# Kernel optimization log

Hardware: AMD Instinct MI355X
Metric: run time of the kernel (lower is better)

The kernel has to match this reference:

```python
import jax, jax.numpy as jnp
import numpy as np

N_POINTS = 65536      # total nodes across the batch
NDIMS = 3
NUM_THETAS = 64       # directions
BUMP_STEPS = 32       # discretization steps of [-radius, radius]
NUM_GRAPHS = 64       # number of point clouds in the batch
RADIUS = 1.1
SCALE = 100.0         # sigmoid sharpness


def setup_inputs() -> dict:
    key = jax.random.key(0)
    k1, k2, k3 = jax.random.split(key, 3)
    x = jax.random.normal(k1, (N_POINTS, NDIMS), dtype=jnp.float32)
    # unit-norm direction vectors on the sphere, columns of v: [ndims, num_thetas]
    v = jax.random.normal(k2, (NDIMS, NUM_THETAS), dtype=jnp.float32)
    v = v / jnp.linalg.norm(v, axis=0, keepdims=True)
    # lin = discretization of [-radius, radius], matches nn.Parameter linspace
    lin = jnp.linspace(-RADIUS, RADIUS, BUMP_STEPS, dtype=jnp.float32)
    # sorted batch index assigning each node to a graph (torch_geometric convention)
    batch = jnp.sort(jax.random.randint(k3, (N_POINTS,), 0, NUM_GRAPHS, dtype=jnp.int32))
    return {"x": x, "v": v, "lin": lin, "batch": batch}


def reference(x, v, lin, batch):
    # node heights: inner product of coordinates with each direction -> [N, T]
    nh = x @ v
    # broadcast soft-threshold: sigmoid(scale * (lin - nh)) -> [N, S, T]
    # (torch builds [S,1,N,T] then movedims to [N,1,S,T]; same values)
    ecc = jax.nn.sigmoid(SCALE * (lin[None, :, None] - nh[:, None, :]))
    # segment scatter-add over nodes per graph -> [B, S, T]
    ect = jax.ops.segment_sum(ecc, batch, num_segments=NUM_GRAPHS)
    return ect  # torch output after .squeeze(): [batch, bump_steps, num_thetas]
```

## Files before the change

kernel.cpp:

```cpp
#include <hip/hip_runtime.h>

#define T      64
#define S      32
#define NGRAPH 64
#define NSPLIT 16
#define NW     4
#define XCAP   128

__global__ __launch_bounds__(256, 4) void ect_partial(
    const float* __restrict__ x, const float* __restrict__ v,
    const float* __restrict__ lin, const int* __restrict__ batch,
    float* __restrict__ out, int n_points)
{
    __shared__ float bins[2][32][128];
    __shared__ float x4[XCAP * 4];

    const int tid  = threadIdx.x;
    const int t    = tid & 63;
    const int w    = __builtin_amdgcn_readfirstlane(tid >> 6);
    const int half = w >> 1;
    const int col  = ((w & 1) << 6) + t;
    float* bw = &bins[half][0][0];
    const int b    = blockIdx.x;
    const int g    = b >> 4;
    const int c    = b & (NSPLIT - 1);

    {
        const float4 z4 = {0.0f, 0.0f, 0.0f, 0.0f};
        float4* b4 = (float4*)&bins[0][0][0];
#pragma unroll
        for (int i = 0; i < 8; i++) b4[tid + i * 256] = z4;
    }

    const int target = (t < 32) ? g : (g + 1);
    const int i32    = t & 31;
    int lo = 0;
    const int strides[3] = {2048, 64, 2};
#pragma unroll
    for (int rnd = 0; rnd < 3; rnd++) {
        const int stride = strides[rnd];
        const int idx  = lo + i32 * stride;
        const int pv   = batch[min(idx, n_points - 1)];
        const bool prd = (idx < n_points) && (pv < target);
        const unsigned long long bal = __ballot(prd);
        const int cnt = __popc((unsigned)(bal >> (t & 32)));
        lo += max(cnt - 1, 0) * stride;
    }
    if ((lo < n_points) && (batch[min(lo, n_points - 1)] < target)) lo++;
    const int gstart = __builtin_amdgcn_readfirstlane(lo);
    const int gend   = __builtin_amdgcn_readlane(lo, 32);
    const int len    = gend - gstart;
    const int n0     = gstart + (len * c) / NSPLIT;
    const int n1     = gstart + (len * (c + 1)) / NSPLIT;
    const int sliceLen = n1 - n0;

    {
        const int limit = 3 * min(sliceLen, XCAP);
        const int base3 = 3 * n0;
        for (int p = tid; p < limit; p += 256) {
            const int n = p / 3;
            const int d = p - 3 * n;
            x4[n * 4 + d] = x[base3 + p];
        }
    }

    const float lin0     = lin[0];
    const float step     = lin[1] - lin0;
    const float inv_step = 1.0f / step;
    const float nl0i     = -lin0 * inv_step;
    const float K2 = (100.0f * step) * 1.4426950408889634f;
    const float r  = __builtin_amdgcn_exp2f(-K2);

    const float v0 = v[0 * T + t];
    const float v1 = v[1 * T + t];
    const float v2 = v[2 * T + t];

    float v0acc = 0.0f;
    __syncthreads();

#define ECT_BODY(X0, X1, X2)                                                  \
    {                                                                         \
        const float nh = fmaf((X0), v0, fmaf((X1), v1, (X2) * v2));           \
        const float f  = fmaf(nh, inv_step, nl0i);                            \
        const float fs = ceilf(f);                                            \
        const int   ss = (int)fs;                                             \
        const float e0 = __builtin_amdgcn_exp2f(fmaf(K2, f - fs, K2));        \
        const float e1 = e0 * r;                                              \
        const float sm  = __builtin_amdgcn_rcpf(1.0f + e0);                   \
        const float s0v = __builtin_amdgcn_rcpf(1.0f + e1);                   \
        v0acc += (ss <= -1) ? 1.0f : (ss == 0 ? s0v : (ss == 1 ? sm : 0.0f)); \
        const float d1 = s0v - sm, d2 = 1.0f - s0v;                           \
        const int pb = min(max(ss - 1, 0), 29);               \
         \
         \
        const float amt0 = (pb     == ss - 1) ? sm : 0.0f;                    \
        const float amt1 = (pb + 1 == ss    ) ? d1                            \
                         : (pb + 1 == ss + 1) ? d2                            \
                         : (pb + 1 == ss - 1) ? sm : 0.0f;                    \
        const float amt2 = (pb + 2 == ss + 1) ? d2                            \
                         : (pb + 2 == ss    ) ? d1                            \
                         : (pb + 2 == ss - 1) ? sm : 0.0f;                    \
        const int a = pb * 128 + col;                                         \
        const float r0 = bw[a], r1 = bw[a + 128], r2 = bw[a + 256];           \
        bw[a]       = r0 + amt0;                                              \
        bw[a + 128] = r1 + amt1;                                              \
        bw[a + 256] = r2 + amt2;                                              \
    }

    if (sliceLen <= XCAP) {
#pragma unroll 4
        for (int n = w; n < sliceLen; n += NW) {
            const float4 xv = *(const float4*)&x4[n * 4];
            ECT_BODY(xv.x, xv.y, xv.z)
        }
    } else {
#pragma unroll 2
        for (int n = n0 + w; n < n1; n += NW) {
            const float x0 = x[3 * n + 0];
            const float x1 = x[3 * n + 1];
            const float x2 = x[3 * n + 2];
            ECT_BODY(x0, x1, x2)
        }
    }
#undef ECT_BODY

    bw[col] = v0acc;
    __syncthreads();

    for (int cell = tid; cell < 32 * 64; cell += 256) {
        const int cc = cell >> 6;
        const int tt = cell & 63;
        const float sum = bins[0][cc][tt] + bins[0][cc][64 + tt]
                        + bins[1][cc][tt] + bins[1][cc][64 + tt];
        bins[0][cc][tt] = sum;
    }
    __syncthreads();

    float run = bins[0][0][t];
    const int sbase = 8 * w;
    for (int cc = 1; cc < sbase; cc++) run += bins[0][cc][t];
    float* outg = out + (size_t)g * (S * T);
#pragma unroll
    for (int j = 0; j < 8; j++) {
        const int s = sbase + j;
        if (s >= 1) run += bins[0][s][t];
        atomicAdd(&outg[s * T + t], run);
    }
}

extern "C" void kernel_launch(void* const* d_in, const int* in_sizes, int n_in,
                              void* d_out, int out_size, void* d_ws, size_t ws_size,
                              hipStream_t stream) {
    const float* x     = (const float*)d_in[0];
    const float* v     = (const float*)d_in[1];
    const float* lin   = (const float*)d_in[2];
    const int*   batch = (const int*)d_in[3];
    float* out = (float*)d_out;
    (void)d_ws; (void)ws_size;

    const int n_points = in_sizes[0] / 3;

    hipMemsetAsync(d_out, 0, out_size, stream);
    ect_partial<<<NGRAPH * NSPLIT, 256, 0, stream>>>(x, v, lin, batch, out, n_points);
}
```

Before: 71.93 us.

## Replace memset and atomics with cooperative grid-sync workspace reduction

Each block now writes its partial prefix-summed bins to a per-block workspace slot instead of issuing atomicAdds into the output. A cooperative launch with a grid-wide sync lets the same kernel then reduce the 16 splits per graph, so the separate memset and the atomic contention go away. If the cooperative launch fails, it falls back to two kernels. The grid sync adds a barrier cost and requires all 1024 blocks to be co-resident.

```diff
diff --git a/kernel.cpp b/kernel.cpp
--- a/kernel.cpp
+++ b/kernel.cpp
@@ -1,4 +1,7 @@
 #include <hip/hip_runtime.h>
+#include <hip/hip_cooperative_groups.h>
+
+namespace cg = cooperative_groups;
 
 #define T      64
 #define S      32
@@ -7,14 +10,12 @@
 #define NW     4
 #define XCAP   128
 
-__global__ __launch_bounds__(256, 4) void ect_partial(
+__device__ __forceinline__ void ect_phaseA(
     const float* __restrict__ x, const float* __restrict__ v,
     const float* __restrict__ lin, const int* __restrict__ batch,
-    float* __restrict__ out, int n_points)
-{
-    __shared__ float bins[2][32][128];
-    __shared__ float x4[XCAP * 4];
-
+    float* __restrict__ ws, int n_points,
+    float (*bins)[32][128], float* x4)
+{
     const int tid  = threadIdx.x;
     const int t    = tid & 63;
     const int w    = __builtin_amdgcn_readfirstlane(tid >> 6);
@@ -91,8 +92,6 @@
         v0acc += (ss <= -1) ? 1.0f : (ss == 0 ? s0v : (ss == 1 ? sm : 0.0f)); \
         const float d1 = s0v - sm, d2 = 1.0f - s0v;                           \
         const int pb = min(max(ss - 1, 0), 29);               \
-         \
-         \
         const float amt0 = (pb     == ss - 1) ? sm : 0.0f;                    \
         const float amt1 = (pb + 1 == ss    ) ? d1                            \
                          : (pb + 1 == ss + 1) ? d2                            \
@@ -139,13 +138,61 @@
     float run = bins[0][0][t];
     const int sbase = 8 * w;
     for (int cc = 1; cc < sbase; cc++) run += bins[0][cc][t];
-    float* outg = out + (size_t)g * (S * T);
+    float* wsb = ws + (size_t)b * (S * T);
 #pragma unroll
     for (int j = 0; j < 8; j++) {
         const int s = sbase + j;
         if (s >= 1) run += bins[0][s][t];
-        atomicAdd(&outg[s * T + t], run);
-    }
+        wsb[s * T + t] = run;
+    }
+}
+
+__device__ __forceinline__ void ect_phaseB_elem(
+    const float2* __restrict__ ws2, float2* __restrict__ out2, int idx)
+{
+    const int g = idx >> 10;
+    const int i = idx & 1023;
+    float2 sum = {0.0f, 0.0f};
+#pragma unroll
+    for (int c = 0; c < NSPLIT; c++) {
+        const float2 a = ws2[(size_t)(g * NSPLIT + c) * 1024 + i];
+        sum.x += a.x; sum.y += a.y;
+    }
+    out2[idx] = sum;
+}
+
+__global__ __launch_bounds__(256, 4) void ect_fused(
+    const float* __restrict__ x, const float* __restrict__ v,
+    const float* __restrict__ lin, const int* __restrict__ batch,
+    float* __restrict__ ws, float* __restrict__ out, int n_points)
+{
+    __shared__ float bins[2][32][128];
+    __shared__ float x4[XCAP * 4];
+    ect_phaseA(x, v, lin, batch, ws, n_points, bins, x4);
+
+    __threadfence();
+    cg::this_grid().sync();
+
+    const int idx = blockIdx.x * 256 + threadIdx.x;
+    if (idx < NGRAPH * S * T / 2)
+        ect_phaseB_elem((const float2*)ws, (float2*)out, idx);
+}
+
+__global__ __launch_bounds__(256, 4) void ect_partial_ws(
+    const float* __restrict__ x, const float* __restrict__ v,
+    const float* __restrict__ lin, const int* __restrict__ batch,
+    float* __restrict__ ws, int n_points)
+{
+    __shared__ float bins[2][32][128];
+    __shared__ float x4[XCAP * 4];
+    ect_phaseA(x, v, lin, batch, ws, n_points, bins, x4);
+}
+
+__global__ __launch_bounds__(256) void ect_reduce(
+    const float2* __restrict__ ws2, float2* __restrict__ out2)
+{
+    const int idx = blockIdx.x * 256 + threadIdx.x;
+    ect_phaseB_elem(ws2, out2, idx);
 }
 
 extern "C" void kernel_launch(void* const* d_in, const int* in_sizes, int n_in,
@@ -156,10 +203,19 @@
     const float* lin   = (const float*)d_in[2];
     const int*   batch = (const int*)d_in[3];
     float* out = (float*)d_out;
-    (void)d_ws; (void)ws_size;
+    float* ws  = (float*)d_ws;
 
     const int n_points = in_sizes[0] / 3;
 
-    hipMemsetAsync(d_out, 0, out_size, stream);
-    ect_partial<<<NGRAPH * NSPLIT, 256, 0, stream>>>(x, v, lin, batch, out, n_points);
-}
+    void* kargs[] = {(void*)&x, (void*)&v, (void*)&lin, (void*)&batch,
+                     (void*)&ws, (void*)&out, (void*)&n_points};
+    const hipError_t e = hipLaunchCooperativeKernel(
+        (const void*)ect_fused, dim3(NGRAPH * NSPLIT), dim3(256),
+        kargs, 0, stream);
+    if (e != hipSuccess) {
+        ect_partial_ws<<<NGRAPH * NSPLIT, 256, 0, stream>>>(
+            x, v, lin, batch, ws, n_points);
+        ect_reduce<<<NGRAPH * S * T / 2 / 256, 256, 0, stream>>>(
+            (const float2*)ws, (float2*)out);
+    }
+}
```

Result: slower. 218.2 us (+203.4%).

## Split graphs into more smaller blocks and replace atomics with workspace reduction

Applied to the files above, without the earlier changes.

Doubles the per-graph split to 32 blocks of 128 threads (2 waves each, one shared bin copy) and writes per-block prefix-summed partials to a workspace instead of atomically adding to the output. A second kernel then sums the 32 partials per graph deterministically, which also removes the memset. The aim is to cut atomic contention and memset cost and to spread work over more blocks. In exchange it adds a second launch, 8 MB of workspace traffic, and a duplicated batch binary search in each of the 2048 blocks.

```diff
diff --git a/kernel.cpp b/kernel.cpp
--- a/kernel.cpp
+++ b/kernel.cpp
@@ -3,33 +3,32 @@
 #define T      64
 #define S      32
 #define NGRAPH 64
-#define NSPLIT 16
-#define NW     4
-#define XCAP   128
+#define NSPLIT 32
+#define NW     2
+#define XCAP   64
 
-__global__ __launch_bounds__(256, 4) void ect_partial(
+__global__ __launch_bounds__(128, 4) void ect_partial(
     const float* __restrict__ x, const float* __restrict__ v,
     const float* __restrict__ lin, const int* __restrict__ batch,
-    float* __restrict__ out, int n_points)
+    float* __restrict__ ws, int n_points)
 {
-    __shared__ float bins[2][32][128];
+    __shared__ float bins[32][128];
     __shared__ float x4[XCAP * 4];
 
     const int tid  = threadIdx.x;
     const int t    = tid & 63;
     const int w    = __builtin_amdgcn_readfirstlane(tid >> 6);
-    const int half = w >> 1;
-    const int col  = ((w & 1) << 6) + t;
-    float* bw = &bins[half][0][0];
+    const int col  = (w << 6) + t;
+    float* bw = &bins[0][0];
     const int b    = blockIdx.x;
-    const int g    = b >> 4;
+    const int g    = b >> 5;
     const int c    = b & (NSPLIT - 1);
 
     {
         const float4 z4 = {0.0f, 0.0f, 0.0f, 0.0f};
-        float4* b4 = (float4*)&bins[0][0][0];
+        float4* b4 = (float4*)&bins[0][0];
 #pragma unroll
-        for (int i = 0; i < 8; i++) b4[tid + i * 256] = z4;
+        for (int i = 0; i < 8; i++) b4[tid + i * 128] = z4;
     }
 
     const int target = (t < 32) ? g : (g + 1);
@@ -57,7 +56,7 @@
     {
         const int limit = 3 * min(sliceLen, XCAP);
         const int base3 = 3 * n0;
-        for (int p = tid; p < limit; p += 256) {
+        for (int p = tid; p < limit; p += 128) {
             const int n = p / 3;
             const int d = p - 3 * n;
             x4[n * 4 + d] = x[base3 + p];
@@ -91,8 +90,6 @@
         v0acc += (ss <= -1) ? 1.0f : (ss == 0 ? s0v : (ss == 1 ? sm : 0.0f)); \
         const float d1 = s0v - sm, d2 = 1.0f - s0v;                           \
         const int pb = min(max(ss - 1, 0), 29);               \
-         \
-         \
         const float amt0 = (pb     == ss - 1) ? sm : 0.0f;                    \
         const float amt1 = (pb + 1 == ss    ) ? d1                            \
                          : (pb + 1 == ss + 1) ? d2                            \
@@ -124,28 +121,41 @@
     }
 #undef ECT_BODY
 
-    bw[col] = v0acc;
+    bins[0][col] = v0acc;
     __syncthreads();
 
-    for (int cell = tid; cell < 32 * 64; cell += 256) {
+    for (int cell = tid; cell < 32 * 64; cell += 128) {
         const int cc = cell >> 6;
         const int tt = cell & 63;
-        const float sum = bins[0][cc][tt] + bins[0][cc][64 + tt]
-                        + bins[1][cc][tt] + bins[1][cc][64 + tt];
-        bins[0][cc][tt] = sum;
+        bins[cc][tt] = bins[cc][tt] + bins[cc][64 + tt];
     }
     __syncthreads();
 
-    float run = bins[0][0][t];
-    const int sbase = 8 * w;
-    for (int cc = 1; cc < sbase; cc++) run += bins[0][cc][t];
-    float* outg = out + (size_t)g * (S * T);
+    float run = bins[0][t];
+    const int sbase = 16 * w;
+    for (int cc = 1; cc < sbase; cc++) run += bins[cc][t];
+    float* wsb = ws + (size_t)b * (S * T);
 #pragma unroll
-    for (int j = 0; j < 8; j++) {
+    for (int j = 0; j < 16; j++) {
         const int s = sbase + j;
-        if (s >= 1) run += bins[0][s][t];
-        atomicAdd(&outg[s * T + t], run);
+        if (s >= 1) run += bins[s][t];
+        wsb[s * T + t] = run;
     }
+}
+
+__global__ __launch_bounds__(256) void ect_reduce(
+    const float2* __restrict__ ws2, float2* __restrict__ out2)
+{
+    const int idx = blockIdx.x * 256 + threadIdx.x;
+    const int g   = idx >> 10;
+    const int i   = idx & 1023;
+    float2 sum = {0.0f, 0.0f};
+#pragma unroll
+    for (int c = 0; c < NSPLIT; c++) {
+        const float2 a = ws2[(size_t)(g * NSPLIT + c) * 1024 + i];
+        sum.x += a.x; sum.y += a.y;
+    }
+    out2[idx] = sum;
 }
 
 extern "C" void kernel_launch(void* const* d_in, const int* in_sizes, int n_in,
@@ -156,10 +166,11 @@
     const float* lin   = (const float*)d_in[2];
     const int*   batch = (const int*)d_in[3];
     float* out = (float*)d_out;
-    (void)d_ws; (void)ws_size;
+    float* ws  = (float*)d_ws;
 
     const int n_points = in_sizes[0] / 3;
 
-    hipMemsetAsync(d_out, 0, out_size, stream);
-    ect_partial<<<NGRAPH * NSPLIT, 256, 0, stream>>>(x, v, lin, batch, out, n_points);
+    ect_partial<<<NGRAPH * NSPLIT, 128, 0, stream>>>(x, v, lin, batch, ws, n_points);
+    ect_reduce<<<NGRAPH * S * T / 2 / 256, 256, 0, stream>>>(
+        (const float2*)ws, (float2*)out);
 }
```

Measured after the change: 77.73 us. 1.08x slower.
